# Kernel tuning notes

Hardware: AMD Instinct MI355X
Metric: run time of the kernel (lower is better)

Reference implementation:

```python
import jax, jax.numpy as jnp
import numpy as np

K_HOPS = 3
ALPHA = 0.3
DELTA = 0.5
KL_EPS = 1e-10
BN_EPS = 1e-5
DEG_MIN = 1e-6

B, T, N, F_IN, H, T_OUT = 8, 12, 1536, 1, 64, 12
HID2 = 2 * H  # MLP hidden width = 128


def setup_inputs() -> dict:
    key = jax.random.key(0)
    ks = jax.random.split(key, 20)
    s = 0.05
    TH = T * H
    inp = {
        "x": jax.random.normal(ks[0], (B, T, N, F_IN), jnp.float32),
        # AdaptiveBiDiffConv weights (stored as (in, out))
        "W1": jax.random.normal(ks[1], (F_IN, H), jnp.float32) * s,
        "W2": jax.random.normal(ks[2], (F_IN, H), jnp.float32) * s,
        # encoder MLPBlock: Linear(TH,128) ReLU Linear(128,128) ReLU Linear(128,64) + proj(TH,64), BN(64)
        "enc_w1": jax.random.normal(ks[3], (TH, HID2), jnp.float32) * s,
        "enc_b1": jnp.zeros((HID2,), jnp.float32),
        "enc_w2": jax.random.normal(ks[4], (HID2, HID2), jnp.float32) * s,
        "enc_b2": jnp.zeros((HID2,), jnp.float32),
        "enc_w3": jax.random.normal(ks[5], (HID2, H), jnp.float32) * s,
        "enc_b3": jnp.zeros((H,), jnp.float32),
        "enc_proj": jax.random.normal(ks[6], (TH, H), jnp.float32) * s,
        "enc_bn_g": jnp.ones((H,), jnp.float32),
        "enc_bn_b": jnp.zeros((H,), jnp.float32),
        "enc_bn_m": jnp.zeros((H,), jnp.float32),
        "enc_bn_v": jnp.ones((H,), jnp.float32),
        # decoder MLPBlock: Linear(64,128) ReLU Linear(128,128) ReLU Linear(128,12) + proj(64,12), BN(12)
        "dec_w1": jax.random.normal(ks[7], (H, HID2), jnp.float32) * s,
        "dec_b1": jnp.zeros((HID2,), jnp.float32),
        "dec_w2": jax.random.normal(ks[8], (HID2, HID2), jnp.float32) * s,
        "dec_b2": jnp.zeros((HID2,), jnp.float32),
        "dec_w3": jax.random.normal(ks[9], (HID2, T_OUT), jnp.float32) * s,
        "dec_b3": jnp.zeros((T_OUT,), jnp.float32),
        "dec_proj": jax.random.normal(ks[10], (H, T_OUT), jnp.float32) * s,
        "dec_bn_g": jnp.ones((T_OUT,), jnp.float32),
        "dec_bn_b": jnp.zeros((T_OUT,), jnp.float32),
        "dec_bn_m": jnp.zeros((T_OUT,), jnp.float32),
        "dec_bn_v": jnp.ones((T_OUT,), jnp.float32),
    }
    return inp


def _row_norm(A):
    return A / jnp.maximum(A.sum(-1, keepdims=True), DEG_MIN)


def _mlp_block(z, w1, b1, w2, b2, w3, b3, proj, g, be, m, v):
    h = jax.nn.relu(z @ w1 + b1)
    h = jax.nn.relu(h @ w2 + b2)
    o = (h @ w3 + b3) + z @ proj
    # BatchNorm1d, eval mode over last (channel) axis
    return (o - m) / jnp.sqrt(v + BN_EPS) * g + be


def _forward(x, W1, W2,
             enc_w1, enc_b1, enc_w2, enc_b2, enc_w3, enc_b3, enc_proj,
             enc_bn_g, enc_bn_b, enc_bn_m, enc_bn_v,
             dec_w1, dec_b1, dec_w2, dec_b2, dec_w3, dec_b3, dec_proj,
             dec_bn_g, dec_bn_b, dec_bn_m, dec_bn_v):
    b, t, n, _ = x.shape
    # ---- KL adjacency (fused form: avoids (B,N,N,T) broadcast) ----
    p = jax.nn.softmax(jnp.transpose(x[..., 0], (0, 2, 1)), axis=-1)  # (B,N,T)
    logp = jnp.log(p + KL_EPS)
    # kl[b,i,j] = sum_t p_i (logp_i - logp_j)
    kl = jnp.sum(p * logp, axis=-1, keepdims=True) - jnp.einsum('bit,bjt->bij', p, logp)
    A = (kl < DELTA).astype(x.dtype)  # (B,N,N)
    A_fwd = _row_norm(A)
    A_bwd = _row_norm(jnp.swapaxes(A, -1, -2))
    # ---- bidirectional diffusion conv (x_k never updated in original loop) ----
    x_flow = x[..., :1]                    # (B,T,N,1)
    x_res = x_flow @ W1                    # (B,T,N,H)
    xw = x_flow @ W2                       # (B,T,N,H)
    fwd = jnp.einsum('bij,btjh->btih', A_fwd, xw)
    bwd = jnp.einsum('bij,btjh->btih', A_bwd, xw)
    x_p = jax.nn.relu(x_res + K_HOPS * (ALPHA * fwd + (1.0 - ALPHA) * bwd))
    # ---- temporal MLP encoder/decoder ----
    x_flat = jnp.transpose(x_p, (0, 2, 1, 3)).reshape(b, n, t * x_p.shape[-1])  # (B,N,T*H)
    x_e = _mlp_block(x_flat, enc_w1, enc_b1, enc_w2, enc_b2, enc_w3, enc_b3,
                     enc_proj, enc_bn_g, enc_bn_b, enc_bn_m, enc_bn_v)  # (B,N,H)
    x_d = _mlp_block(x_e, dec_w1, dec_b1, dec_w2, dec_b2, dec_w3, dec_b3,
                     dec_proj, dec_bn_g, dec_bn_b, dec_bn_m, dec_bn_v)  # (B,N,T_out)
    return jnp.transpose(x_d, (0, 2, 1))[..., None]  # (B,T_out,N,1)


def reference(x, W1, W2,
              enc_w1, enc_b1, enc_w2, enc_b2, enc_w3, enc_b3, enc_proj,
              enc_bn_g, enc_bn_b, enc_bn_m, enc_bn_v,
              dec_w1, dec_b1, dec_w2, dec_b2, dec_w3, dec_b3, dec_proj,
              dec_bn_g, dec_bn_b, dec_bn_m, dec_bn_v):
    return _forward(x, W1, W2,
                    enc_w1, enc_b1, enc_w2, enc_b2, enc_w3, enc_b3, enc_proj,
                    enc_bn_g, enc_bn_b, enc_bn_m, enc_bn_v,
                    dec_w1, dec_b1, dec_w2, dec_b2, dec_w3, dec_b3, dec_proj,
                    dec_bn_g, dec_bn_b, dec_bn_m, dec_bn_v)
```

## Files before the change

kernel.cpp:

```cpp
#include <hip/hip_runtime.h>
#include <hip/hip_bf16.h>


namespace {

constexpr int Bn = 8, Nn = 1536, TOUT = 12;
constexpr int Mrows = Bn * Nn;
constexpr int JS = 8;

typedef __attribute__((ext_vector_type(8))) short bf8;
typedef __attribute__((ext_vector_type(4))) float f4;
typedef unsigned short ush;

__device__ __forceinline__ float b2f(__hip_bfloat16 v) { return __bfloat162float(v); }
__device__ __forceinline__ ush f2bu(float f) {
  union { __hip_bfloat16 h; ush u; } c; c.h = __float2bfloat16(f); return c.u;
}
__device__ __forceinline__ float bu2f(ush u) {
  union { unsigned int i; float f; } c; c.i = ((unsigned)u) << 16; return c.f;
}
__device__ __forceinline__ float ldraw(const void* p, size_t i, int fl) {
  return fl ? ((const float*)p)[i] : b2f(((const __hip_bfloat16*)p)[i]);
}

__device__ __forceinline__ int detect_fl(const void* x, int tid) {
  __shared__ int cnt;
  if (tid == 0) cnt = 0;
  __syncthreads();
  const ush* u = (const ush*)x;
  int c = 0;
#pragma unroll
  for (int s = 0; s < 16; ++s) {
    ush v = u[tid + s * 256];
    if (((v >> 7) & 0xFF) >= 140) c++;
  }
  atomicAdd(&cnt, c);
  __syncthreads();
  return (cnt > 64) ? 1 : 0;
}

struct SmallTab { const void* src[16]; int n[16]; int off[16]; };
struct RepTab { const void* src[8]; int Nc[8]; int NCT[8]; int lb[9]; };

__global__ __launch_bounds__(256) void prep_all(
    const void* __restrict__ xraw, SmallTab st, RepTab rt,
    int* __restrict__ flag, float* __restrict__ CS,
    float* __restrict__ xT, float* __restrict__ sd,
    ush* __restrict__ pA, ush* __restrict__ lA,
    ush* __restrict__ phi16, ush* __restrict__ plo16,
    ush* __restrict__ lhi16, ush* __restrict__ llo16,
    ush* __restrict__ Xc, ush* __restrict__ Wf) {
  int tid = threadIdx.x;
  int fl = detect_fl(xraw, tid);
  int blk = blockIdx.x;

  if (blk < 48) {
    int row = blk * 256 + tid;
    int b = row / Nn, n = row - b * Nn;
    float xv[12];
#pragma unroll
    for (int t = 0; t < 12; ++t)
      xv[t] = ldraw(xraw, (size_t)(b * 12 + t) * Nn + n, fl);
    float mx = xv[0];
#pragma unroll
    for (int t = 1; t < 12; ++t) mx = fmaxf(mx, xv[t]);
    float e[12], Z = 0.f;
#pragma unroll
    for (int t = 0; t < 12; ++t) { e[t] = expf(xv[t] - mx); Z += e[t]; }
    float invZ = 1.f / Z;
    float sacc = 0.f;
    ush pa[32], la[32], ph[16], pl[16], lh[16], ll[16];
#pragma unroll
    for (int k = 0; k < 32; ++k) { pa[k] = 0; la[k] = 0; }
#pragma unroll
    for (int k = 0; k < 16; ++k) { ph[k] = 0; pl[k] = 0; lh[k] = 0; ll[k] = 0; }
#pragma unroll
    for (int t = 0; t < 12; ++t) {
      float pv = e[t] * invZ;
      float lv = logf(pv + 1e-10f);
      sacc += pv * lv;
      xT[(size_t)row * 12 + t] = xv[t];
      ush phv = f2bu(pv);  float plv = pv - bu2f(phv);
      ush lhv = f2bu(lv);  float llv = lv - bu2f(lhv);
      pa[t] = phv; pa[16 + t] = f2bu(plv);
      la[t] = lhv; la[16 + t] = f2bu(llv);
      ph[t] = phv; pl[t] = f2bu(plv);
      lh[t] = lhv; ll[t] = f2bu(llv);
      Xc[((size_t)(b * 16 + t)) * Nn + n] = f2bu(xv[t]);
    }
    Xc[((size_t)(b * 16 + 12)) * Nn + n] = 0x3F80;
#pragma unroll
    for (int t = 13; t < 16; ++t) Xc[((size_t)(b * 16 + t)) * Nn + n] = 0;
    sd[row] = sacc;
    {
      uint4* d = (uint4*)(pA + (size_t)row * 32);
      const uint4* s = (const uint4*)pa;
      d[0] = s[0]; d[1] = s[1]; d[2] = s[2]; d[3] = s[3];
      uint4* d2 = (uint4*)(lA + (size_t)row * 32);
      const uint4* s2 = (const uint4*)la;
      d2[0] = s2[0]; d2[1] = s2[1]; d2[2] = s2[2]; d2[3] = s2[3];
      ((uint4*)(phi16 + (size_t)row * 16))[0] = ((const uint4*)ph)[0];
      ((uint4*)(phi16 + (size_t)row * 16))[1] = ((const uint4*)ph)[1];
      ((uint4*)(plo16 + (size_t)row * 16))[0] = ((const uint4*)pl)[0];
      ((uint4*)(plo16 + (size_t)row * 16))[1] = ((const uint4*)pl)[1];
      ((uint4*)(lhi16 + (size_t)row * 16))[0] = ((const uint4*)lh)[0];
      ((uint4*)(lhi16 + (size_t)row * 16))[1] = ((const uint4*)lh)[1];
      ((uint4*)(llo16 + (size_t)row * 16))[0] = ((const uint4*)ll)[0];
      ((uint4*)(llo16 + (size_t)row * 16))[1] = ((const uint4*)ll)[1];
    }
  } else if (blk < 146) {
    int idx = (blk - 48) * 256 + tid;
    if (idx >= rt.lb[8]) return;
    int mi = 0;
#pragma unroll
    for (int i = 1; i < 8; ++i) if (idx >= rt.lb[i]) mi = i;
    int li = idx - rt.lb[mi];
    int NCT = rt.NCT[mi], Nc = rt.Nc[mi];
    int per = NCT * 64;
    int c0 = li / per, rem = li - c0 * per;
    int ct = rem >> 6, l = rem & 63;
    int q = l >> 4, m = l & 15;
    int col = ct * 16 + m;
    ush* d = Wf + (size_t)idx * 8;
#pragma unroll
    for (int j = 0; j < 8; ++j) {
      int k = c0 * 32 + q * 8 + j;
      d[j] = (col < Nc) ? f2bu(ldraw(rt.src[mi], (size_t)k * Nc + col, fl)) : 0;
    }
  } else {
    for (int i = 0; i < 16; ++i)
      for (int e = tid; e < st.n[i]; e += 256)
        CS[st.off[i] + e] = ldraw(st.src[i], e, fl);
    if (tid == 0) flag[0] = fl;
  }
}

__global__ __launch_bounds__(256) void kl_mfma(
    const ush* __restrict__ pA, const ush* __restrict__ lA,
    const ush* __restrict__ phi16, const ush* __restrict__ plo16,
    const ush* __restrict__ lhi16, const ush* __restrict__ llo16,
    const ush* __restrict__ Xc, const float* __restrict__ sd,
    float* __restrict__ psf, float* __restrict__ psb) {
  __shared__ ush T1[4][512], T2[4][512];
  int tid = threadIdx.x, w = tid >> 6, l = tid & 63, q = l >> 4, n = l & 15;
  int blk = blockIdx.x;
  int b = blk / 192, rem = blk % 192, ig = rem >> 3, js = rem & 7;
  int i0 = ig * 64 + w * 16;
  int rowb = b * Nn;

  bf8 z8 = {0, 0, 0, 0, 0, 0, 0, 0};
  bf8 aP = *(const bf8*)(pA + ((size_t)(rowb + i0 + n)) * 32 + q * 8);
  bf8 aL = *(const bf8*)(lA + ((size_t)(rowb + i0 + n)) * 32 + q * 8);
  bf8 aPh = (q < 2) ? aP : z8;
  bf8 aLh = (q < 2) ? aL : z8;
  float selfI[4];
#pragma unroll
  for (int r = 0; r < 4; ++r) selfI[r] = sd[rowb + i0 + q * 4 + r];

  f4 accF = {0.f, 0.f, 0.f, 0.f}, accB = {0.f, 0.f, 0.f, 0.f};

  for (int jp = 0; jp < 6; ++jp) {
    int jl = js * 192 + jp * 32;
#pragma unroll
    for (int hh = 0; hh < 2; ++hh) {
      int jh = jl + hh * 16;
      size_t bb = ((size_t)(rowb + jh + n)) * 16 + (q & 1) * 8;
      bf8 bLh = *(const bf8*)(lhi16 + bb);
      bf8 bLo = *(const bf8*)(llo16 + bb);
      bf8 bPh = *(const bf8*)(phi16 + bb);
      bf8 bPo = *(const bf8*)(plo16 + bb);
      float selfJ = sd[rowb + jh + n];

      f4 s1 = {0.f, 0.f, 0.f, 0.f}, s2 = {0.f, 0.f, 0.f, 0.f};
      s1 = __builtin_amdgcn_mfma_f32_16x16x32_bf16(aP, bLh, s1, 0, 0, 0);
      s1 = __builtin_amdgcn_mfma_f32_16x16x32_bf16(aPh, bLo, s1, 0, 0, 0);
      s2 = __builtin_amdgcn_mfma_f32_16x16x32_bf16(aL, bPh, s2, 0, 0, 0);
      s2 = __builtin_amdgcn_mfma_f32_16x16x32_bf16(aLh, bPo, s2, 0, 0, 0);

      int qk = n >> 3, kj = n & 7;
#pragma unroll
      for (int r = 0; r < 4; ++r) {
        int pos = hh * 256 + (qk * 16 + q * 4 + r) * 8 + kj;
        T1[w][pos] = (selfI[r] - s1[r] < 0.5f) ? (ush)0x3F80 : (ush)0;
        T2[w][pos] = (selfJ - s2[r] < 0.5f) ? (ush)0x3F80 : (ush)0;
      }
    }
    bf8 af1 = *(const bf8*)(&T1[w][(size_t)l * 8]);
    bf8 af2 = *(const bf8*)(&T2[w][(size_t)l * 8]);
    bf8 xfr = *(const bf8*)(Xc + ((size_t)(b * 16 + n)) * Nn + jl + q * 8);
    accF = __builtin_amdgcn_mfma_f32_16x16x32_bf16(af1, xfr, accF, 0, 0, 0);
    accB = __builtin_amdgcn_mfma_f32_16x16x32_bf16(af2, xfr, accB, 0, 0, 0);
  }
#pragma unroll
  for (int r = 0; r < 4; ++r) {
    size_t o = ((size_t)js * Mrows + rowb + i0 + q * 4 + r) * 16 + n;
    psf[o] = accF[r];
    psb[o] = accB[r];
  }
}

__global__ __launch_bounds__(256) void fused_mlp(
    const float* __restrict__ xT,
    const float* __restrict__ psf, const float* __restrict__ psb,
    const float* __restrict__ CS, const ush* __restrict__ Wf,
    const int* __restrict__ flag, void* __restrict__ outp) {
  __shared__ float xs[16][12], ccs[16][12];
  __shared__ float sfs[16][16], sbs[16][16];
  __shared__ float ws1[64], ws2[64];
  __shared__ ush hf[2048], hg[2048], xf[1024];
  __shared__ ush zf[12288];
  __shared__ f4 red[4][64];

  int tid = threadIdx.x, w = tid >> 6, l = tid & 63, q = l >> 4, n = l & 15;
  int r0 = blockIdx.x * 16;

  {
    int r = tid >> 4, t = tid & 15;
    float a = 0.f, b = 0.f;
#pragma unroll
    for (int js = 0; js < JS; ++js) {
      size_t o = ((size_t)js * Mrows + r0 + r) * 16 + t;
      a += psf[o];
      b += psb[o];
    }
    sfs[r][t] = a;
    sbs[r][t] = b;
    if (tid < 128) { if (tid < 64) ws1[tid] = CS[tid]; else ws2[tid - 64] = CS[tid]; }
    if (tid < 192) {
      int rr = tid / 12, tt = tid - rr * 12;
      xs[rr][tt] = xT[(size_t)(r0 + rr) * 12 + tt];
    }
  }
  __syncthreads();
  if (tid < 192) {
    int rr = tid / 12, tt = tid - rr * 12;
    float irs = 1.f / fmaxf(sfs[rr][12], 1e-6f);
    float ics = 1.f / fmaxf(sbs[rr][12], 1e-6f);
    ccs[rr][tt] = 3.0f * (0.3f * sfs[rr][tt] * irs + 0.7f * sbs[rr][tt] * ics);
  }
  __syncthreads();

  auto zregen = [&](int c0) -> bf8 {
    int t = c0 >> 1, h0 = (c0 & 1) * 32 + q * 8;
    float xv = xs[n][t], cv = ccs[n][t];
    union { bf8 v; ush u[8]; } au;
#pragma unroll
    for (int j = 0; j < 8; ++j)
      au.u[j] = f2bu(fmaxf(fmaf(xv, ws1[h0 + j], cv * ws2[h0 + j]), 0.f));
    return au.v;
  };
  auto fpos = [&](int ct, int r) -> int {
    return ((ct >> 1) * 64 + ((ct & 1) * 2 + (n >> 3)) * 16 + q * 4 + r) * 8 + (n & 7);
  };

#pragma unroll
  for (int u = 0; u < 6; ++u) {
    int c0 = w * 6 + u;
    bf8 v = zregen(c0);
    *(bf8*)(&zf[((size_t)c0 * 64 + l) * 8]) = v;
  }
  __syncthreads();

  {
    f4 a0 = {0.f, 0.f, 0.f, 0.f}, a1 = {0.f, 0.f, 0.f, 0.f};
    for (int c0 = 0; c0 < 24; ++c0) {
      bf8 a = *(const bf8*)(&zf[((size_t)c0 * 64 + l) * 8]);
      const ush* wb = Wf + ((size_t)(c0 * 8 + 2 * w) * 64 + l) * 8;
      bf8 b0 = *(const bf8*)wb;
      bf8 b1 = *(const bf8*)(wb + 512);
      a0 = __builtin_amdgcn_mfma_f32_16x16x32_bf16(a, b0, a0, 0, 0, 0);
      a1 = __builtin_amdgcn_mfma_f32_16x16x32_bf16(a, b1, a1, 0, 0, 0);
    }
#pragma unroll
    for (int u2 = 0; u2 < 2; ++u2) {
      int ct = 2 * w + u2;
      f4 acc = u2 ? a1 : a0;
      float bz = CS[128 + ct * 16 + n];
#pragma unroll
      for (int r = 0; r < 4; ++r)
        hf[fpos(ct, r)] = f2bu(fmaxf(acc[r] + bz, 0.f));
    }
  }
  __syncthreads();

  {
    f4 a0 = {0.f, 0.f, 0.f, 0.f}, a1 = {0.f, 0.f, 0.f, 0.f};
    for (int c0 = 0; c0 < 4; ++c0) {
      bf8 a = *(const bf8*)(&hf[(size_t)(c0 * 64 + l) * 8]);
      const ush* wb = Wf + 98304 + ((size_t)(c0 * 8 + 2 * w) * 64 + l) * 8;
      bf8 b0 = *(const bf8*)wb;
      bf8 b1 = *(const bf8*)(wb + 512);
      a0 = __builtin_amdgcn_mfma_f32_16x16x32_bf16(a, b0, a0, 0, 0, 0);
      a1 = __builtin_amdgcn_mfma_f32_16x16x32_bf16(a, b1, a1, 0, 0, 0);
    }
    __syncthreads();
#pragma unroll
    for (int u2 = 0; u2 < 2; ++u2) {
      int ct = 2 * w + u2;
      f4 acc = u2 ? a1 : a0;
      float bz = CS[256 + ct * 16 + n];
#pragma unroll
      for (int r = 0; r < 4; ++r)
        hg[fpos(ct, r)] = f2bu(fmaxf(acc[r] + bz, 0.f));
    }
  }
  __syncthreads();

  {
    f4 a3 = {0.f, 0.f, 0.f, 0.f};
    for (int c0 = 0; c0 < 4; ++c0) {
      bf8 a = *(const bf8*)(&hg[(size_t)(c0 * 64 + l) * 8]);
      bf8 b = *(const bf8*)(Wf + 114688 + ((size_t)(c0 * 4 + w) * 64 + l) * 8);
      a3 = __builtin_amdgcn_mfma_f32_16x16x32_bf16(a, b, a3, 0, 0, 0);
    }
    for (int c0 = 0; c0 < 24; ++c0) {
      bf8 a = *(const bf8*)(&zf[((size_t)c0 * 64 + l) * 8]);
      bf8 b = *(const bf8*)(Wf + 122880 + ((size_t)(c0 * 4 + w) * 64 + l) * 8);
      a3 = __builtin_amdgcn_mfma_f32_16x16x32_bf16(a, b, a3, 0, 0, 0);
    }
    int col = w * 16 + n;
    float g = CS[448 + col], be = CS[512 + col], mm = CS[576 + col], vv = CS[640 + col];
    float sc = g / sqrtf(vv + 1e-5f);
    float sh = be - mm * sc;
    float bz = CS[384 + col];
#pragma unroll
    for (int r = 0; r < 4; ++r)
      xf[fpos(w, r)] = f2bu((a3[r] + bz) * sc + sh);
  }
  __syncthreads();

  {
    f4 a0 = {0.f, 0.f, 0.f, 0.f}, a1 = {0.f, 0.f, 0.f, 0.f};
    for (int c0 = 0; c0 < 2; ++c0) {
      bf8 a = *(const bf8*)(&xf[(size_t)(c0 * 64 + l) * 8]);
      const ush* wb = Wf + 172032 + ((size_t)(c0 * 8 + 2 * w) * 64 + l) * 8;
      bf8 b0 = *(const bf8*)wb;
      bf8 b1 = *(const bf8*)(wb + 512);
      a0 = __builtin_amdgcn_mfma_f32_16x16x32_bf16(a, b0, a0, 0, 0, 0);
      a1 = __builtin_amdgcn_mfma_f32_16x16x32_bf16(a, b1, a1, 0, 0, 0);
    }
    __syncthreads();
#pragma unroll
    for (int u2 = 0; u2 < 2; ++u2) {
      int ct = 2 * w + u2;
      f4 acc = u2 ? a1 : a0;
      float bz = CS[704 + ct * 16 + n];
#pragma unroll
      for (int r = 0; r < 4; ++r)
        hf[fpos(ct, r)] = f2bu(fmaxf(acc[r] + bz, 0.f));
    }
  }
  __syncthreads();

  {
    f4 a0 = {0.f, 0.f, 0.f, 0.f}, a1 = {0.f, 0.f, 0.f, 0.f};
    for (int c0 = 0; c0 < 4; ++c0) {
      bf8 a = *(const bf8*)(&hf[(size_t)(c0 * 64 + l) * 8]);
      const ush* wb = Wf + 180224 + ((size_t)(c0 * 8 + 2 * w) * 64 + l) * 8;
      bf8 b0 = *(const bf8*)wb;
      bf8 b1 = *(const bf8*)(wb + 512);
      a0 = __builtin_amdgcn_mfma_f32_16x16x32_bf16(a, b0, a0, 0, 0, 0);
      a1 = __builtin_amdgcn_mfma_f32_16x16x32_bf16(a, b1, a1, 0, 0, 0);
    }
    __syncthreads();
#pragma unroll
    for (int u2 = 0; u2 < 2; ++u2) {
      int ct = 2 * w + u2;
      f4 acc = u2 ? a1 : a0;
      float bz = CS[832 + ct * 16 + n];
#pragma unroll
      for (int r = 0; r < 4; ++r)
        hg[fpos(ct, r)] = f2bu(fmaxf(acc[r] + bz, 0.f));
    }
  }
  __syncthreads();

  {
    f4 ao = {0.f, 0.f, 0.f, 0.f};
    {
      bf8 a = *(const bf8*)(&hg[(size_t)(w * 64 + l) * 8]);
      bf8 b = *(const bf8*)(Wf + 196608 + ((size_t)w * 64 + l) * 8);
      ao = __builtin_amdgcn_mfma_f32_16x16x32_bf16(a, b, ao, 0, 0, 0);
    }
    if (w < 2) {
      bf8 a = *(const bf8*)(&xf[(size_t)(w * 64 + l) * 8]);
      bf8 b = *(const bf8*)(Wf + 198656 + ((size_t)w * 64 + l) * 8);
      ao = __builtin_amdgcn_mfma_f32_16x16x32_bf16(a, b, ao, 0, 0, 0);
    }
    red[w][l] = ao;
  }
  __syncthreads();
  if (w == 0) {
    f4 s = red[0][l] + red[1][l] + red[2][l] + red[3][l];
    int fl = flag[0];
    if (n < 12) {
      float bz = CS[960 + n];
      float g = CS[972 + n], be = CS[984 + n], mm = CS[996 + n], vv = CS[1008 + n];
      float sc = g / sqrtf(vv + 1e-5f);
      float sh = be - mm * sc;
#pragma unroll
      for (int r = 0; r < 4; ++r) {
        int row = r0 + q * 4 + r;
        int bb = row / Nn, nn = row - bb * Nn;
        size_t oi = ((size_t)bb * TOUT + n) * Nn + nn;
        float ov = (s[r] + bz) * sc + sh;
        if (fl) ((float*)outp)[oi] = ov;
        else    ((ush*)outp)[oi] = f2bu(ov);
      }
    }
  }
}

}

extern "C" void kernel_launch(void* const* d_in, const int* in_sizes, int n_in,
                              void* d_out, int out_size, void* d_ws, size_t ws_size,
                              hipStream_t stream) {
  float* f = (float*)d_ws;
  int* flag = (int*)d_ws;
  float* CS  = f + 16;
  float* xT  = f + 1040;
  float* sd  = f + 148496;
  float* psf = f + 160784;
  float* psb = f + 1733648;
  ush* U = (ush*)(f + 3306512);
  ush* pA    = U;
  ush* lA    = U + 393216;
  ush* phi16 = U + 786432;
  ush* plo16 = U + 983040;
  ush* lhi16 = U + 1179648;
  ush* llo16 = U + 1376256;
  ush* Xc    = U + 1572864;
  ush* Wf    = U + 1769472;

  SmallTab st;
  {
    const int idxs[16] = {1, 2, 4, 6, 8, 10, 11, 12, 13, 15, 17, 19, 21, 22, 23, 24};
    const int ns[16]   = {64, 64, 128, 128, 64, 64, 64, 64, 64, 128, 128, 12, 12, 12, 12, 12};
    int off = 0;
    for (int i = 0; i < 16; ++i) {
      st.src[i] = d_in[idxs[i]]; st.n[i] = ns[i]; st.off[i] = off; off += ns[i];
    }
  }
  RepTab rt;
  {
    const int idxs[8]  = {3, 5, 7, 9, 14, 16, 18, 20};
    const int rNc[8]   = {128, 128, 64, 64, 128, 128, 12, 12};
    const int rNCT[8]  = {8, 8, 4, 4, 8, 8, 1, 1};
    const int rlb[9]   = {0, 12288, 14336, 15360, 21504, 22528, 24576, 24832, 24960};
    for (int i = 0; i < 8; ++i) {
      rt.src[i] = d_in[idxs[i]]; rt.Nc[i] = rNc[i]; rt.NCT[i] = rNCT[i];
    }
    for (int i = 0; i < 9; ++i) rt.lb[i] = rlb[i];
  }

  prep_all<<<147, 256, 0, stream>>>(d_in[0], st, rt, flag, CS, xT, sd,
                                    pA, lA, phi16, plo16, lhi16, llo16, Xc, Wf);
  kl_mfma<<<1536, 256, 0, stream>>>(pA, lA, phi16, plo16, lhi16, llo16,
                                    Xc, sd, psf, psb);
  fused_mlp<<<768, 256, 0, stream>>>(xT, psf, psb, CS, Wf, flag, d_out);
}
```

Measured before the change: 148.9 us.

## Fuse prep, KL-mask and MLP kernels into one persistent kernel with grid barrier

Merges the three launches into one 768-block kernel. Each block first does its share of preprocessing, then all blocks meet at an atomic grid-wide barrier. After the barrier each block computes its 16 rows' KL-masked diffusion, with its 4 waves splitting the j range and reducing through shared memory, and runs the MLP directly. This removes the psf/psb partial-sum round trip through global memory, the xT buffer and two launch overheads. In exchange the preprocessing runs with far fewer threads per block, and the spin barrier relies on all 768 blocks being co-resident (launch bounds of 3 blocks per CU), otherwise it deadlocks.

```diff
diff --git a/kernel.cpp b/kernel.cpp
--- a/kernel.cpp
+++ b/kernel.cpp
@@ -4,9 +4,7 @@
 
 namespace {
 
-constexpr int Bn = 8, Nn = 1536, TOUT = 12;
-constexpr int Mrows = Bn * Nn;
-constexpr int JS = 8;
+constexpr int Nn = 1536, TOUT = 12;
 
 typedef __attribute__((ext_vector_type(8))) short bf8;
 typedef __attribute__((ext_vector_type(4))) float f4;
@@ -42,25 +40,35 @@
 struct SmallTab { const void* src[16]; int n[16]; int off[16]; };
 struct RepTab { const void* src[8]; int Nc[8]; int NCT[8]; int lb[9]; };
 
-__global__ __launch_bounds__(256) void prep_all(
+__global__ __launch_bounds__(256, 3) void mega(
     const void* __restrict__ xraw, SmallTab st, RepTab rt,
-    int* __restrict__ flag, float* __restrict__ CS,
-    float* __restrict__ xT, float* __restrict__ sd,
+    int* __restrict__ bar, float* __restrict__ CS,
+    float* __restrict__ sd,
     ush* __restrict__ pA, ush* __restrict__ lA,
     ush* __restrict__ phi16, ush* __restrict__ plo16,
     ush* __restrict__ lhi16, ush* __restrict__ llo16,
-    ush* __restrict__ Xc, ush* __restrict__ Wf) {
-  int tid = threadIdx.x;
+    ush* __restrict__ Xc, ush* __restrict__ Wf,
+    void* __restrict__ outp) {
+  __shared__ float xs[16][12], ccs[16][12];
+  __shared__ float sfs[16][16], sbs[16][16];
+  __shared__ float ws1[64], ws2[64];
+  __shared__ ush hf[2048], hg[2048], xf[1024];
+  __shared__ f4 red[4][64], red2[4][64];
+  __shared__ union { ush T[2][4][512]; ush zf[12288]; } u;
+
+  int tid = threadIdx.x, w = tid >> 6, l = tid & 63, q = l >> 4, n = l & 15;
+  int bi = blockIdx.x;
   int fl = detect_fl(xraw, tid);
-  int blk = blockIdx.x;
-
-  if (blk < 48) {
-    int row = blk * 256 + tid;
-    int b = row / Nn, n = row - b * Nn;
+  int r0 = bi * 16;
+  int b = bi / 96;
+  int rowb = b * Nn;
+
+  if (tid < 16) {
+    int r = r0 + tid, nn = r - rowb;
     float xv[12];
 #pragma unroll
     for (int t = 0; t < 12; ++t)
-      xv[t] = ldraw(xraw, (size_t)(b * 12 + t) * Nn + n, fl);
+      xv[t] = ldraw(xraw, (size_t)(b * 12 + t) * Nn + nn, fl);
     float mx = xv[0];
 #pragma unroll
     for (int t = 1; t < 12; ++t) mx = fmaxf(mx, xv[t]);
@@ -79,157 +87,139 @@
       float pv = e[t] * invZ;
       float lv = logf(pv + 1e-10f);
       sacc += pv * lv;
-      xT[(size_t)row * 12 + t] = xv[t];
+      xs[tid][t] = xv[t];
       ush phv = f2bu(pv);  float plv = pv - bu2f(phv);
       ush lhv = f2bu(lv);  float llv = lv - bu2f(lhv);
       pa[t] = phv; pa[16 + t] = f2bu(plv);
       la[t] = lhv; la[16 + t] = f2bu(llv);
       ph[t] = phv; pl[t] = f2bu(plv);
       lh[t] = lhv; ll[t] = f2bu(llv);
-      Xc[((size_t)(b * 16 + t)) * Nn + n] = f2bu(xv[t]);
-    }
-    Xc[((size_t)(b * 16 + 12)) * Nn + n] = 0x3F80;
-#pragma unroll
-    for (int t = 13; t < 16; ++t) Xc[((size_t)(b * 16 + t)) * Nn + n] = 0;
-    sd[row] = sacc;
+      Xc[((size_t)(b * 16 + t)) * Nn + nn] = f2bu(xv[t]);
+    }
+    Xc[((size_t)(b * 16 + 12)) * Nn + nn] = 0x3F80;
+#pragma unroll
+    for (int t = 13; t < 16; ++t) Xc[((size_t)(b * 16 + t)) * Nn + nn] = 0;
+    sd[r] = sacc;
     {
-      uint4* d = (uint4*)(pA + (size_t)row * 32);
+      uint4* d = (uint4*)(pA + (size_t)r * 32);
       const uint4* s = (const uint4*)pa;
       d[0] = s[0]; d[1] = s[1]; d[2] = s[2]; d[3] = s[3];
-      uint4* d2 = (uint4*)(lA + (size_t)row * 32);
+      uint4* d2 = (uint4*)(lA + (size_t)r * 32);
       const uint4* s2 = (const uint4*)la;
       d2[0] = s2[0]; d2[1] = s2[1]; d2[2] = s2[2]; d2[3] = s2[3];
-      ((uint4*)(phi16 + (size_t)row * 16))[0] = ((const uint4*)ph)[0];
-      ((uint4*)(phi16 + (size_t)row * 16))[1] = ((const uint4*)ph)[1];
-      ((uint4*)(plo16 + (size_t)row * 16))[0] = ((const uint4*)pl)[0];
-      ((uint4*)(plo16 + (size_t)row * 16))[1] = ((const uint4*)pl)[1];
-      ((uint4*)(lhi16 + (size_t)row * 16))[0] = ((const uint4*)lh)[0];
-      ((uint4*)(lhi16 + (size_t)row * 16))[1] = ((const uint4*)lh)[1];
-      ((uint4*)(llo16 + (size_t)row * 16))[0] = ((const uint4*)ll)[0];
-      ((uint4*)(llo16 + (size_t)row * 16))[1] = ((const uint4*)ll)[1];
-    }
-  } else if (blk < 146) {
-    int idx = (blk - 48) * 256 + tid;
-    if (idx >= rt.lb[8]) return;
-    int mi = 0;
-#pragma unroll
-    for (int i = 1; i < 8; ++i) if (idx >= rt.lb[i]) mi = i;
-    int li = idx - rt.lb[mi];
-    int NCT = rt.NCT[mi], Nc = rt.Nc[mi];
-    int per = NCT * 64;
-    int c0 = li / per, rem = li - c0 * per;
-    int ct = rem >> 6, l = rem & 63;
-    int q = l >> 4, m = l & 15;
-    int col = ct * 16 + m;
-    ush* d = Wf + (size_t)idx * 8;
-#pragma unroll
-    for (int j = 0; j < 8; ++j) {
-      int k = c0 * 32 + q * 8 + j;
-      d[j] = (col < Nc) ? f2bu(ldraw(rt.src[mi], (size_t)k * Nc + col, fl)) : 0;
-    }
+      ((uint4*)(phi16 + (size_t)r * 16))[0] = ((const uint4*)ph)[0];
+      ((uint4*)(phi16 + (size_t)r * 16))[1] = ((const uint4*)ph)[1];
+      ((uint4*)(plo16 + (size_t)r * 16))[0] = ((const uint4*)pl)[0];
+      ((uint4*)(plo16 + (size_t)r * 16))[1] = ((const uint4*)pl)[1];
+      ((uint4*)(lhi16 + (size_t)r * 16))[0] = ((const uint4*)lh)[0];
+      ((uint4*)(lhi16 + (size_t)r * 16))[1] = ((const uint4*)lh)[1];
+      ((uint4*)(llo16 + (size_t)r * 16))[0] = ((const uint4*)ll)[0];
+      ((uint4*)(llo16 + (size_t)r * 16))[1] = ((const uint4*)ll)[1];
+    }
+  } else if (tid >= 64 && tid < 97) {
+    int idx = bi * 33 + (tid - 64);
+    if (idx < rt.lb[8]) {
+      int mi = 0;
+#pragma unroll
+      for (int i = 1; i < 8; ++i) if (idx >= rt.lb[i]) mi = i;
+      int li = idx - rt.lb[mi];
+      int NCT = rt.NCT[mi], Nc = rt.Nc[mi];
+      int per = NCT * 64;
+      int c0 = li / per, rem = li - c0 * per;
+      int ct = rem >> 6, lq = rem & 63;
+      int qq = lq >> 4, m = lq & 15;
+      int col = ct * 16 + m;
+      ush* d = Wf + (size_t)idx * 8;
+#pragma unroll
+      for (int j = 0; j < 8; ++j) {
+        int k = c0 * 32 + qq * 8 + j;
+        d[j] = (col < Nc) ? f2bu(ldraw(rt.src[mi], (size_t)k * Nc + col, fl)) : 0;
+      }
+    }
+  } else if (tid >= 128 && tid < 136 && bi < 128) {
+    int e = bi * 8 + (tid - 128);
+    if (e < 1020) {
+      int i = 0;
+#pragma unroll
+      for (int k = 1; k < 16; ++k) if (e >= st.off[k]) i = k;
+      CS[e] = ldraw(st.src[i], e - st.off[i], fl);
+    }
+  }
+
+  __syncthreads();
+  if (tid == 0) {
+    __threadfence();
+    int arr = atomicAdd(bar, 1);
+    if (arr == 767) {
+      atomicExch(bar + 1, 1);
+    } else {
+      while (atomicAdd(bar + 1, 0) == 0) __builtin_amdgcn_s_sleep(8);
+    }
+    __threadfence();
+  }
+  __syncthreads();
+
+  {
+    bf8 z8 = {0, 0, 0, 0, 0, 0, 0, 0};
+    bf8 aP = *(const bf8*)(pA + ((size_t)(r0 + n)) * 32 + q * 8);
+    bf8 aL = *(const bf8*)(lA + ((size_t)(r0 + n)) * 32 + q * 8);
+    bf8 aPh = (q < 2) ? aP : z8;
+    bf8 aLh = (q < 2) ? aL : z8;
+    float selfI[4];
+#pragma unroll
+    for (int r = 0; r < 4; ++r) selfI[r] = sd[r0 + q * 4 + r];
+
+    f4 accF = {0.f, 0.f, 0.f, 0.f}, accB = {0.f, 0.f, 0.f, 0.f};
+
+    for (int jp = 0; jp < 12; ++jp) {
+      int jl = w * 384 + jp * 32;
+#pragma unroll
+      for (int hh = 0; hh < 2; ++hh) {
+        int jh = jl + hh * 16;
+        size_t bb = ((size_t)(rowb + jh + n)) * 16 + (q & 1) * 8;
+        bf8 bLh = *(const bf8*)(lhi16 + bb);
+        bf8 bLo = *(const bf8*)(llo16 + bb);
+        bf8 bPh = *(const bf8*)(phi16 + bb);
+        bf8 bPo = *(const bf8*)(plo16 + bb);
+        float selfJ = sd[rowb + jh + n];
+
+        f4 s1 = {0.f, 0.f, 0.f, 0.f}, s2 = {0.f, 0.f, 0.f, 0.f};
+        s1 = __builtin_amdgcn_mfma_f32_16x16x32_bf16(aP, bLh, s1, 0, 0, 0);
+        s1 = __builtin_amdgcn_mfma_f32_16x16x32_bf16(aPh, bLo, s1, 0, 0, 0);
+        s2 = __builtin_amdgcn_mfma_f32_16x16x32_bf16(aL, bPh, s2, 0, 0, 0);
+        s2 = __builtin_amdgcn_mfma_f32_16x16x32_bf16(aLh, bPo, s2, 0, 0, 0);
+
+        int qk = n >> 3, kj = n & 7;
+#pragma unroll
+        for (int r = 0; r < 4; ++r) {
+          int pos = hh * 256 + (qk * 16 + q * 4 + r) * 8 + kj;
+          u.T[0][w][pos] = (selfI[r] - s1[r] < 0.5f) ? (ush)0x3F80 : (ush)0;
+          u.T[1][w][pos] = (selfJ - s2[r] < 0.5f) ? (ush)0x3F80 : (ush)0;
+        }
+      }
+      bf8 af1 = *(const bf8*)(&u.T[0][w][(size_t)l * 8]);
+      bf8 af2 = *(const bf8*)(&u.T[1][w][(size_t)l * 8]);
+      bf8 xfr = *(const bf8*)(Xc + ((size_t)(b * 16 + n)) * Nn + jl + q * 8);
+      accF = __builtin_amdgcn_mfma_f32_16x16x32_bf16(af1, xfr, accF, 0, 0, 0);
+      accB = __builtin_amdgcn_mfma_f32_16x16x32_bf16(af2, xfr, accB, 0, 0, 0);
+    }
+    red[w][l] = accF;
+    red2[w][l] = accB;
+  }
+  __syncthreads();
+
+  if (w == 0) {
+    f4 s = red[0][l] + red[1][l] + red[2][l] + red[3][l];
+#pragma unroll
+    for (int r = 0; r < 4; ++r) sfs[q * 4 + r][n] = s[r];
+  } else if (w == 1) {
+    f4 s = red2[0][l] + red2[1][l] + red2[2][l] + red2[3][l];
+#pragma unroll
+    for (int r = 0; r < 4; ++r) sbs[q * 4 + r][n] = s[r];
+  } else if (w == 2) {
+    ws1[l] = CS[l];
   } else {
-    for (int i = 0; i < 16; ++i)
-      for (int e = tid; e < st.n[i]; e += 256)
-        CS[st.off[i] + e] = ldraw(st.src[i], e, fl);
-    if (tid == 0) flag[0] = fl;
-  }
-}
-
-__global__ __launch_bounds__(256) void kl_mfma(
-    const ush* __restrict__ pA, const ush* __restrict__ lA,
-    const ush* __restrict__ phi16, const ush* __restrict__ plo16,
-    const ush* __restrict__ lhi16, const ush* __restrict__ llo16,
-    const ush* __restrict__ Xc, const float* __restrict__ sd,
-    float* __restrict__ psf, float* __restrict__ psb) {
-  __shared__ ush T1[4][512], T2[4][512];
-  int tid = threadIdx.x, w = tid >> 6, l = tid & 63, q = l >> 4, n = l & 15;
-  int blk = blockIdx.x;
-  int b = blk / 192, rem = blk % 192, ig = rem >> 3, js = rem & 7;
-  int i0 = ig * 64 + w * 16;
-  int rowb = b * Nn;
-
-  bf8 z8 = {0, 0, 0, 0, 0, 0, 0, 0};
-  bf8 aP = *(const bf8*)(pA + ((size_t)(rowb + i0 + n)) * 32 + q * 8);
-  bf8 aL = *(const bf8*)(lA + ((size_t)(rowb + i0 + n)) * 32 + q * 8);
-  bf8 aPh = (q < 2) ? aP : z8;
-  bf8 aLh = (q < 2) ? aL : z8;
-  float selfI[4];
-#pragma unroll
-  for (int r = 0; r < 4; ++r) selfI[r] = sd[rowb + i0 + q * 4 + r];
-
-  f4 accF = {0.f, 0.f, 0.f, 0.f}, accB = {0.f, 0.f, 0.f, 0.f};
-
-  for (int jp = 0; jp < 6; ++jp) {
-    int jl = js * 192 + jp * 32;
-#pragma unroll
-    for (int hh = 0; hh < 2; ++hh) {
-      int jh = jl + hh * 16;
-      size_t bb = ((size_t)(rowb + jh + n)) * 16 + (q & 1) * 8;
-      bf8 bLh = *(const bf8*)(lhi16 + bb);
-      bf8 bLo = *(const bf8*)(llo16 + bb);
-      bf8 bPh = *(const bf8*)(phi16 + bb);
-      bf8 bPo = *(const bf8*)(plo16 + bb);
-      float selfJ = sd[rowb + jh + n];
-
-      f4 s1 = {0.f, 0.f, 0.f, 0.f}, s2 = {0.f, 0.f, 0.f, 0.f};
-      s1 = __builtin_amdgcn_mfma_f32_16x16x32_bf16(aP, bLh, s1, 0, 0, 0);
-      s1 = __builtin_amdgcn_mfma_f32_16x16x32_bf16(aPh, bLo, s1, 0, 0, 0);
-      s2 = __builtin_amdgcn_mfma_f32_16x16x32_bf16(aL, bPh, s2, 0, 0, 0);
-      s2 = __builtin_amdgcn_mfma_f32_16x16x32_bf16(aLh, bPo, s2, 0, 0, 0);
-
-      int qk = n >> 3, kj = n & 7;
-#pragma unroll
-      for (int r = 0; r < 4; ++r) {
-        int pos = hh * 256 + (qk * 16 + q * 4 + r) * 8 + kj;
-        T1[w][pos] = (selfI[r] - s1[r] < 0.5f) ? (ush)0x3F80 : (ush)0;
-        T2[w][pos] = (selfJ - s2[r] < 0.5f) ? (ush)0x3F80 : (ush)0;
-      }
-    }
-    bf8 af1 = *(const bf8*)(&T1[w][(size_t)l * 8]);
-    bf8 af2 = *(const bf8*)(&T2[w][(size_t)l * 8]);
-    bf8 xfr = *(const bf8*)(Xc + ((size_t)(b * 16 + n)) * Nn + jl + q * 8);
-    accF = __builtin_amdgcn_mfma_f32_16x16x32_bf16(af1, xfr, accF, 0, 0, 0);
-    accB = __builtin_amdgcn_mfma_f32_16x16x32_bf16(af2, xfr, accB, 0, 0, 0);
-  }
-#pragma unroll
-  for (int r = 0; r < 4; ++r) {
-    size_t o = ((size_t)js * Mrows + rowb + i0 + q * 4 + r) * 16 + n;
-    psf[o] = accF[r];
-    psb[o] = accB[r];
-  }
-}
-
-__global__ __launch_bounds__(256) void fused_mlp(
-    const float* __restrict__ xT,
-    const float* __restrict__ psf, const float* __restrict__ psb,
-    const float* __restrict__ CS, const ush* __restrict__ Wf,
-    const int* __restrict__ flag, void* __restrict__ outp) {
-  __shared__ float xs[16][12], ccs[16][12];
-  __shared__ float sfs[16][16], sbs[16][16];
-  __shared__ float ws1[64], ws2[64];
-  __shared__ ush hf[2048], hg[2048], xf[1024];
-  __shared__ ush zf[12288];
-  __shared__ f4 red[4][64];
-
-  int tid = threadIdx.x, w = tid >> 6, l = tid & 63, q = l >> 4, n = l & 15;
-  int r0 = blockIdx.x * 16;
-
-  {
-    int r = tid >> 4, t = tid & 15;
-    float a = 0.f, b = 0.f;
-#pragma unroll
-    for (int js = 0; js < JS; ++js) {
-      size_t o = ((size_t)js * Mrows + r0 + r) * 16 + t;
-      a += psf[o];
-      b += psb[o];
-    }
-    sfs[r][t] = a;
-    sbs[r][t] = b;
-    if (tid < 128) { if (tid < 64) ws1[tid] = CS[tid]; else ws2[tid - 64] = CS[tid]; }
-    if (tid < 192) {
-      int rr = tid / 12, tt = tid - rr * 12;
-      xs[rr][tt] = xT[(size_t)(r0 + rr) * 12 + tt];
-    }
+    ws2[l] = CS[64 + l];
   }
   __syncthreads();
   if (tid < 192) {
@@ -243,10 +233,10 @@
   auto zregen = [&](int c0) -> bf8 {
     int t = c0 >> 1, h0 = (c0 & 1) * 32 + q * 8;
     float xv = xs[n][t], cv = ccs[n][t];
-    union { bf8 v; ush u[8]; } au;
+    union { bf8 v; ush uu[8]; } au;
 #pragma unroll
     for (int j = 0; j < 8; ++j)
-      au.u[j] = f2bu(fmaxf(fmaf(xv, ws1[h0 + j], cv * ws2[h0 + j]), 0.f));
+      au.uu[j] = f2bu(fmaxf(fmaf(xv, ws1[h0 + j], cv * ws2[h0 + j]), 0.f));
     return au.v;
   };
   auto fpos = [&](int ct, int r) -> int {
@@ -254,17 +244,17 @@
   };
 
 #pragma unroll
-  for (int u = 0; u < 6; ++u) {
-    int c0 = w * 6 + u;
+  for (int u6 = 0; u6 < 6; ++u6) {
+    int c0 = w * 6 + u6;
     bf8 v = zregen(c0);
-    *(bf8*)(&zf[((size_t)c0 * 64 + l) * 8]) = v;
+    *(bf8*)(&u.zf[((size_t)c0 * 64 + l) * 8]) = v;
   }
   __syncthreads();
 
   {
     f4 a0 = {0.f, 0.f, 0.f, 0.f}, a1 = {0.f, 0.f, 0.f, 0.f};
     for (int c0 = 0; c0 < 24; ++c0) {
-      bf8 a = *(const bf8*)(&zf[((size_t)c0 * 64 + l) * 8]);
+      bf8 a = *(const bf8*)(&u.zf[((size_t)c0 * 64 + l) * 8]);
       const ush* wb = Wf + ((size_t)(c0 * 8 + 2 * w) * 64 + l) * 8;
       bf8 b0 = *(const bf8*)wb;
       bf8 b1 = *(const bf8*)(wb + 512);
@@ -310,13 +300,13 @@
     f4 a3 = {0.f, 0.f, 0.f, 0.f};
     for (int c0 = 0; c0 < 4; ++c0) {
       bf8 a = *(const bf8*)(&hg[(size_t)(c0 * 64 + l) * 8]);
-      bf8 b = *(const bf8*)(Wf + 114688 + ((size_t)(c0 * 4 + w) * 64 + l) * 8);
-      a3 = __builtin_amdgcn_mfma_f32_16x16x32_bf16(a, b, a3, 0, 0, 0);
+      bf8 bb = *(const bf8*)(Wf + 114688 + ((size_t)(c0 * 4 + w) * 64 + l) * 8);
+      a3 = __builtin_amdgcn_mfma_f32_16x16x32_bf16(a, bb, a3, 0, 0, 0);
     }
     for (int c0 = 0; c0 < 24; ++c0) {
-      bf8 a = *(const bf8*)(&zf[((size_t)c0 * 64 + l) * 8]);
-      bf8 b = *(const bf8*)(Wf + 122880 + ((size_t)(c0 * 4 + w) * 64 + l) * 8);
-      a3 = __builtin_amdgcn_mfma_f32_16x16x32_bf16(a, b, a3, 0, 0, 0);
+      bf8 a = *(const bf8*)(&u.zf[((size_t)c0 * 64 + l) * 8]);
+      bf8 bb = *(const bf8*)(Wf + 122880 + ((size_t)(c0 * 4 + w) * 64 + l) * 8);
+      a3 = __builtin_amdgcn_mfma_f32_16x16x32_bf16(a, bb, a3, 0, 0, 0);
     }
     int col = w * 16 + n;
     float g = CS[448 + col], be = CS[512 + col], mm = CS[576 + col], vv = CS[640 + col];
@@ -379,20 +369,19 @@
     f4 ao = {0.f, 0.f, 0.f, 0.f};
     {
       bf8 a = *(const bf8*)(&hg[(size_t)(w * 64 + l) * 8]);
-      bf8 b = *(const bf8*)(Wf + 196608 + ((size_t)w * 64 + l) * 8);
-      ao = __builtin_amdgcn_mfma_f32_16x16x32_bf16(a, b, ao, 0, 0, 0);
+      bf8 bb = *(const bf8*)(Wf + 196608 + ((size_t)w * 64 + l) * 8);
+      ao = __builtin_amdgcn_mfma_f32_16x16x32_bf16(a, bb, ao, 0, 0, 0);
     }
     if (w < 2) {
       bf8 a = *(const bf8*)(&xf[(size_t)(w * 64 + l) * 8]);
-      bf8 b = *(const bf8*)(Wf + 198656 + ((size_t)w * 64 + l) * 8);
-      ao = __builtin_amdgcn_mfma_f32_16x16x32_bf16(a, b, ao, 0, 0, 0);
+      bf8 bb = *(const bf8*)(Wf + 198656 + ((size_t)w * 64 + l) * 8);
+      ao = __builtin_amdgcn_mfma_f32_16x16x32_bf16(a, bb, ao, 0, 0, 0);
     }
     red[w][l] = ao;
   }
   __syncthreads();
   if (w == 0) {
     f4 s = red[0][l] + red[1][l] + red[2][l] + red[3][l];
-    int fl = flag[0];
     if (n < 12) {
       float bz = CS[960 + n];
       float g = CS[972 + n], be = CS[984 + n], mm = CS[996 + n], vv = CS[1008 + n];
@@ -401,8 +390,8 @@
 #pragma unroll
       for (int r = 0; r < 4; ++r) {
         int row = r0 + q * 4 + r;
-        int bb = row / Nn, nn = row - bb * Nn;
-        size_t oi = ((size_t)bb * TOUT + n) * Nn + nn;
+        int bb2 = row / Nn, nn2 = row - bb2 * Nn;
+        size_t oi = ((size_t)bb2 * TOUT + n) * Nn + nn2;
         float ov = (s[r] + bz) * sc + sh;
         if (fl) ((float*)outp)[oi] = ov;
         else    ((ush*)outp)[oi] = f2bu(ov);
@@ -417,13 +406,10 @@
                               void* d_out, int out_size, void* d_ws, size_t ws_size,
                               hipStream_t stream) {
   float* f = (float*)d_ws;
-  int* flag = (int*)d_ws;
+  int* bar   = (int*)d_ws;
   float* CS  = f + 16;
-  float* xT  = f + 1040;
-  float* sd  = f + 148496;
-  float* psf = f + 160784;
-  float* psb = f + 1733648;
-  ush* U = (ush*)(f + 3306512);
+  float* sd  = f + 1040;
+  ush* U = (ush*)(f + 13328);
   ush* pA    = U;
   ush* lA    = U + 393216;
   ush* phi16 = U + 786432;
@@ -454,9 +440,8 @@
     for (int i = 0; i < 9; ++i) rt.lb[i] = rlb[i];
   }
 
-  prep_all<<<147, 256, 0, stream>>>(d_in[0], st, rt, flag, CS, xT, sd,
-                                    pA, lA, phi16, plo16, lhi16, llo16, Xc, Wf);
-  kl_mfma<<<1536, 256, 0, stream>>>(pA, lA, phi16, plo16, lhi16, llo16,
-                                    Xc, sd, psf, psb);
-  fused_mlp<<<768, 256, 0, stream>>>(xT, psf, psb, CS, Wf, flag, d_out);
-}
+  hipMemsetAsync(d_ws, 0, 16, stream);
+  mega<<<768, 256, 0, stream>>>(d_in[0], st, rt, bar, CS, sd,
+                                pA, lA, phi16, plo16, lhi16, llo16,
+                                Xc, Wf, d_out);
+}
```

Measured after the change: 199.4 us. 1.34x slower.
